# Optimization experiments

Measured on AMD Instinct MI355X. Metric: run time of the kernel, lower is better.

## Reference

```python
import jax, jax.numpy as jnp
import numpy as np

D_MODEL = 320
N_HEADS = 8
D_HEADS = 40
D_COND = 768
D_ATTN = N_HEADS * D_HEADS  # 320


def setup_inputs() -> dict:
    key = jax.random.key(0)
    ks = jax.random.split(key, 7)
    B, S, SK = 2, 4096, 4096
    x = jax.random.normal(ks[0], (B, S, D_MODEL), dtype=jnp.float32)
    cond = jax.random.normal(ks[1], (B, SK, D_COND), dtype=jnp.float32)
    # Linear weights stored as [in, out]; torch nn.Linear(in, out) has W [out, in],
    # applied as x @ W.T, equivalent to x @ W_here.
    sq = 1.0 / np.sqrt(D_MODEL)
    sc = 1.0 / np.sqrt(D_COND)
    sa = 1.0 / np.sqrt(D_ATTN)
    Wq = jax.random.uniform(ks[2], (D_MODEL, D_ATTN), jnp.float32, -sq, sq)
    Wk = jax.random.uniform(ks[3], (D_COND, D_ATTN), jnp.float32, -sc, sc)
    Wv = jax.random.uniform(ks[4], (D_COND, D_ATTN), jnp.float32, -sc, sc)
    Wo = jax.random.uniform(ks[5], (D_ATTN, D_MODEL), jnp.float32, -sa, sa)
    bo = jax.random.uniform(ks[6], (D_MODEL,), jnp.float32, -sa, sa)
    return {"x": x, "cond": cond, "Wq": Wq, "Wk": Wk, "Wv": Wv, "Wo": Wo, "bo": bo}


def reference(x, cond, Wq, Wk, Wv, Wo, bo):
    B, S, _ = x.shape
    SK = cond.shape[1]
    scale = D_HEADS ** -0.5
    q = (x @ Wq).reshape(B, S, N_HEADS, D_HEADS)      # [B,S,H,Dh]
    k = (cond @ Wk).reshape(B, SK, N_HEADS, D_HEADS)  # [B,SK,H,Dh]
    v = (cond @ Wv).reshape(B, SK, N_HEADS, D_HEADS)
    # materialized O(N^2) scores, as in the source (einsum -> softmax -> einsum)
    attn = jnp.einsum('bihd,bjhd->bhij', q, k) * scale  # [B,H,S,SK]
    attn = jax.nn.softmax(attn, axis=-1)
    out = jnp.einsum('bhij,bjhd->bihd', attn, v)        # [B,S,H,Dh]
    out = out.reshape(B, S, D_ATTN)
    return out @ Wo + bo
```

## Files before the change

### kernel.cpp

```cpp
#include <hip/hip_runtime.h>

typedef __attribute__((ext_vector_type(8))) short s16x8;
typedef __attribute__((ext_vector_type(4))) short s16x4;
typedef __attribute__((ext_vector_type(8))) __bf16 bf16x8;
typedef __attribute__((ext_vector_type(4))) float f32x4;
typedef __attribute__((ext_vector_type(4))) unsigned short u16x4;
typedef __attribute__((ext_vector_type(4))) unsigned int u32x4;

__device__ __forceinline__ f32x4 mfma_bf16(s16x8 a, s16x8 b, f32x4 c) {
  return __builtin_amdgcn_mfma_f32_16x16x32_bf16(
      __builtin_bit_cast(bf16x8, a), __builtin_bit_cast(bf16x8, b), c, 0, 0, 0);
}

__device__ __forceinline__ unsigned short f2bf(float f) {
  unsigned int u = __builtin_bit_cast(unsigned int, f);
  unsigned int r = u + 0x7FFFu + ((u >> 16) & 1u);
  return (unsigned short)(r >> 16);
}

__device__ __forceinline__ unsigned int cvt_pk_bf16(float lo, float hi) {
  unsigned int d;
  asm volatile("v_cvt_pk_bf16_f32 %0, %1, %2" : "=v"(d) : "v"(lo), "v"(hi));
  return d;
}

__global__ __launch_bounds__(256) void f32_to_bf16(const float* __restrict__ in,
                                                   unsigned short* __restrict__ out,
                                                   int n4) {
  int i = blockIdx.x * 256 + threadIdx.x;
  if (i < n4) {
    f32x4 v = ((const f32x4*)in)[i];
    u16x4 o;
    o[0] = f2bf(v[0]); o[1] = f2bf(v[1]); o[2] = f2bf(v[2]); o[3] = f2bf(v[3]);
    ((u16x4*)out)[i] = o;
  }
}

__global__ void transpose_f32_bf16(const float* __restrict__ in,
                                   unsigned short* __restrict__ out, int K, int N) {
  int id = blockIdx.x * 256 + threadIdx.x;
  if (id < K * N) {
    int k = id / N, n = id - k * N;
    out[(size_t)n * K + k] = f2bf(in[id]);
  }
}

template <int MODE, int K>
__global__ __launch_bounds__(256) void gemm_direct(
    const unsigned short* __restrict__ A, const unsigned short* __restrict__ Wt,
    void* __restrict__ dstv, const float* __restrict__ bias, float scale) {
  const int tid = threadIdx.x;
  const int l = tid & 63, w = tid >> 6;
  const int wm = w >> 1, wn = w & 1;
  const int lr = l & 15, lg = l >> 4;
  const int row0 = blockIdx.x * 64 + wm * 32;
  const int col0 = blockIdx.y * 64 + wn * 32;

  const unsigned short* Ap = A + (size_t)(row0 + lr) * K + lg * 8;
  const unsigned short* Bp = Wt + (size_t)(col0 + lr) * K + lg * 8;

  f32x4 acc[2][2];
#pragma unroll
  for (int i = 0; i < 2; i++)
#pragma unroll
    for (int j = 0; j < 2; j++) acc[i][j] = f32x4{0.f, 0.f, 0.f, 0.f};

  constexpr int NB = K / 32;
  s16x8 a0[2], a1[2], b0[2], b1[2];
  a0[0] = *(const s16x8*)(Ap);
  a1[0] = *(const s16x8*)(Ap + (size_t)16 * K);
  b0[0] = *(const s16x8*)(Bp);
  b1[0] = *(const s16x8*)(Bp + (size_t)16 * K);

#pragma unroll
  for (int i = 0; i < NB; i++) {
    const int cur = i & 1, nxt = cur ^ 1;
    if (i + 1 < NB) {
      const int k = (i + 1) * 32;
      a0[nxt] = *(const s16x8*)(Ap + k);
      a1[nxt] = *(const s16x8*)(Ap + (size_t)16 * K + k);
      b0[nxt] = *(const s16x8*)(Bp + k);
      b1[nxt] = *(const s16x8*)(Bp + (size_t)16 * K + k);
    }
    acc[0][0] = mfma_bf16(a0[cur], b0[cur], acc[0][0]);
    acc[0][1] = mfma_bf16(a0[cur], b1[cur], acc[0][1]);
    acc[1][0] = mfma_bf16(a1[cur], b0[cur], acc[1][0]);
    acc[1][1] = mfma_bf16(a1[cur], b1[cur], acc[1][1]);
  }

#pragma unroll
  for (int mf = 0; mf < 2; mf++)
#pragma unroll
    for (int nf = 0; nf < 2; nf++)
#pragma unroll
      for (int r = 0; r < 4; r++) {
        int m = row0 + mf * 16 + lg * 4 + r;
        int n = col0 + nf * 16 + lr;
        float v = acc[mf][nf][r];
        if (MODE == 0 || MODE == 1) {
          int b = m >> 12, s = m & 4095;
          int h = n / 40, d = n - h * 40;
          ((unsigned short*)dstv)[((size_t)(b * 8 + h) * 4096 + s) * 64 + d] =
              f2bf(v * scale);
        } else if (MODE == 2) {
          int b = m >> 12, s = m & 4095;
          int h = n / 40, d = n - h * 40;
          ((unsigned short*)dstv)[((size_t)(b * 8 + h) * 48 + d) * 4096 + s] = f2bf(v);
        } else {
          ((float*)dstv)[(size_t)m * 320 + n] = v + bias[n];
        }
      }
}

__global__ __launch_bounds__(512) void attn_kernel(
    const unsigned short* __restrict__ Qh, const unsigned short* __restrict__ Kh,
    const unsigned short* __restrict__ Vt, unsigned short* __restrict__ AO) {
  __shared__ __align__(16) char kt[8192];
  __shared__ __align__(16) char vts[6144];

  const int tid = threadIdx.x;
  const int l = tid & 63, w = tid >> 6;
  const int lr = l & 15, lg = l >> 4;
  const int bh = blockIdx.y;
  const int b = bh >> 3, h = bh & 7;
  const int qbase = blockIdx.x * 128;
  const int qrow = qbase + w * 16 + lr;

  const unsigned short* Qp = Qh + ((size_t)bh * 4096 + qbase + w * 16) * 64;
  const unsigned short* Kp = Kh + (size_t)bh * 4096 * 64;
  const unsigned short* Vp = Vt + (size_t)bh * 48 * 4096;

  const int srow = tid >> 3, sch = tid & 7;
  const bool hasv = (tid < 384);
  const int kofs = ((srow * 128 + sch * 16) ^ ((srow & 7) << 4));

  s16x8 q0 = *(const s16x8*)(Qp + lr * 64 + lg * 8);
  s16x8 q1 = *(const s16x8*)(Qp + lr * 64 + 32 + lg * 8);

  f32x4 O[3];
#pragma unroll
  for (int nf = 0; nf < 3; nf++) O[nf] = f32x4{0.f, 0.f, 0.f, 0.f};
  float rm = -1e30f, rl = 0.f;

  s16x8 kreg = *(const s16x8*)(Kp + (size_t)srow * 64 + sch * 8);
  s16x8 vreg;
  if (hasv) vreg = *(const s16x8*)(Vp + (size_t)srow * 4096 + sch * 8);
  *(s16x8*)(kt + kofs) = kreg;
  if (hasv) *(s16x8*)(vts + kofs) = vreg;
  __syncthreads();

  for (int kb = 0; kb < 4096; kb += 64) {
    if (kb + 64 < 4096) {
      kreg = *(const s16x8*)(Kp + (size_t)(kb + 64 + srow) * 64 + sch * 8);
      if (hasv) vreg = *(const s16x8*)(Vp + (size_t)srow * 4096 + kb + 64 + sch * 8);
    }

    f32x4 sf[4];
#pragma unroll
    for (int nf = 0; nf < 4; nf++) sf[nf] = f32x4{0.f, 0.f, 0.f, 0.f};
    __builtin_amdgcn_s_setprio(1);
#pragma unroll
    for (int nf = 0; nf < 4; nf++) {
      int krow = nf * 16 + lr;
      s16x8 kf0 = *(const s16x8*)(kt + ((krow * 128 + lg * 16) ^ ((krow & 7) << 4)));
      s16x8 kf1 = *(const s16x8*)(kt + ((krow * 128 + 64 + lg * 16) ^ ((krow & 7) << 4)));
      sf[nf] = mfma_bf16(kf0, q0, sf[nf]);
      sf[nf] = mfma_bf16(kf1, q1, sf[nf]);
    }
    __builtin_amdgcn_s_setprio(0);

    float tm = fmaxf(fmaxf(fmaxf(sf[0][0], sf[0][1]), fmaxf(sf[0][2], sf[0][3])),
                     fmaxf(fmaxf(sf[1][0], sf[1][1]), fmaxf(sf[1][2], sf[1][3])));
    tm = fmaxf(tm, fmaxf(fmaxf(fmaxf(sf[2][0], sf[2][1]), fmaxf(sf[2][2], sf[2][3])),
                         fmaxf(fmaxf(sf[3][0], sf[3][1]), fmaxf(sf[3][2], sf[3][3]))));
    tm = fmaxf(tm, __shfl_xor(tm, 16, 64));
    tm = fmaxf(tm, __shfl_xor(tm, 32, 64));
    if (!__all(tm <= rm)) {
      float mn = fmaxf(rm, tm);
      float al = __builtin_amdgcn_exp2f(rm - mn);
      rm = mn;
      rl *= al;
#pragma unroll
      for (int nf = 0; nf < 3; nf++) {
#pragma unroll
        for (int r = 0; r < 4; r++) O[nf][r] *= al;
      }
    }
    float ts = 0.f;
    unsigned int pk[4][2];
#pragma unroll
    for (int nf = 0; nf < 4; nf++) {
      float p0 = __builtin_amdgcn_exp2f(sf[nf][0] - rm);
      float p1 = __builtin_amdgcn_exp2f(sf[nf][1] - rm);
      float p2 = __builtin_amdgcn_exp2f(sf[nf][2] - rm);
      float p3 = __builtin_amdgcn_exp2f(sf[nf][3] - rm);
      ts += (p0 + p1) + (p2 + p3);
      pk[nf][0] = cvt_pk_bf16(p0, p1);
      pk[nf][1] = cvt_pk_bf16(p2, p3);
    }
    ts += __shfl_xor(ts, 16, 64);
    ts += __shfl_xor(ts, 32, 64);
    rl += ts;

    __builtin_amdgcn_s_setprio(1);
#pragma unroll
    for (int c = 0; c < 2; c++) {
      u32x4 bu = {pk[2 * c][0], pk[2 * c][1], pk[2 * c + 1][0], pk[2 * c + 1][1]};
      s16x8 bfrag = __builtin_bit_cast(s16x8, bu);
#pragma unroll
      for (int nf = 0; nf < 3; nf++) {
        int row = nf * 16 + lr;
        int base = row * 128 + c * 64 + lg * 8;
        int swz = (row & 7) << 4;
        s16x4 a0 = *(const s16x4*)(vts + ((base) ^ swz));
        s16x4 a1 = *(const s16x4*)(vts + ((base + 32) ^ swz));
        s16x8 afrag = {a0[0], a0[1], a0[2], a0[3], a1[0], a1[1], a1[2], a1[3]};
        O[nf] = mfma_bf16(afrag, bfrag, O[nf]);
      }
    }
    __builtin_amdgcn_s_setprio(0);

    __syncthreads();
    if (kb + 64 < 4096) {
      *(s16x8*)(kt + kofs) = kreg;
      if (hasv) *(s16x8*)(vts + kofs) = vreg;
    }
    __syncthreads();
  }

  float inv = 1.f / rl;
#pragma unroll
  for (int nf = 0; nf < 3; nf++) {
#pragma unroll
    for (int r = 0; r < 4; r++) {
      int d = nf * 16 + lg * 4 + r;
      if (d < 40) {
        AO[((size_t)(b * 4096 + qrow)) * 320 + h * 40 + d] = f2bf(O[nf][r] * inv);
      }
    }
  }
}

extern "C" void kernel_launch(void* const* d_in, const int* in_sizes, int n_in,
                              void* d_out, int out_size, void* d_ws,
                              size_t ws_size, hipStream_t stream) {
  const float* x    = (const float*)d_in[0];
  const float* cond = (const float*)d_in[1];
  const float* Wq   = (const float*)d_in[2];
  const float* Wk   = (const float*)d_in[3];
  const float* Wv   = (const float*)d_in[4];
  const float* Wo   = (const float*)d_in[5];
  const float* bo   = (const float*)d_in[6];

  char* ws = (char*)d_ws;
  unsigned short* xb    = (unsigned short*)(ws + 0);
  unsigned short* condb = (unsigned short*)(ws + 5242880);
  unsigned short* WtQ   = (unsigned short*)(ws + 17825792);
  unsigned short* WtK   = (unsigned short*)(ws + 18030592);
  unsigned short* WtV   = (unsigned short*)(ws + 18522112);
  unsigned short* WtO   = (unsigned short*)(ws + 19013632);
  unsigned short* AO    = (unsigned short*)(ws + 19218432);
  unsigned short* Qh    = (unsigned short*)(ws + 24461312);
  unsigned short* Kh    = (unsigned short*)(ws + 32849920);
  unsigned short* Vt    = (unsigned short*)(ws + 41238528);

  hipMemsetAsync(Qh, 0, 23068672, stream);

  f32_to_bf16<<<dim3(2560), 256, 0, stream>>>(x, xb, 655360);
  f32_to_bf16<<<dim3(6144), 256, 0, stream>>>(cond, condb, 1572864);

  transpose_f32_bf16<<<dim3(400), 256, 0, stream>>>(Wq, WtQ, 320, 320);
  transpose_f32_bf16<<<dim3(960), 256, 0, stream>>>(Wk, WtK, 768, 320);
  transpose_f32_bf16<<<dim3(960), 256, 0, stream>>>(Wv, WtV, 768, 320);
  transpose_f32_bf16<<<dim3(400), 256, 0, stream>>>(Wo, WtO, 320, 320);

  const float qscale = 1.44269504088896f / sqrtf(40.0f);

  gemm_direct<0, 320><<<dim3(128, 5), 256, 0, stream>>>(xb, WtQ, Qh, nullptr, qscale);
  gemm_direct<1, 768><<<dim3(128, 5), 256, 0, stream>>>(condb, WtK, Kh, nullptr, 1.0f);
  gemm_direct<2, 768><<<dim3(128, 5), 256, 0, stream>>>(condb, WtV, Vt, nullptr, 1.0f);

  attn_kernel<<<dim3(32, 16), 512, 0, stream>>>(Qh, Kh, Vt, AO);

  gemm_direct<3, 320><<<dim3(128, 5), 256, 0, stream>>>(AO, WtO, d_out, bo, 1.0f);
}
```

Measured before the change: 294.9 us.

## Double-buffer attention K/V tiles, permute V layout, and merge small launches

The attention loop now ping-pongs between two LDS buffers for K and V, so the next tile is written while the current one is read, and each iteration needs one barrier instead of two. V columns are stored in a permuted sequence order so the PV operand loads as a single 16-byte LDS read rather than two 8-byte reads plus a shuffle. The conversion, transpose and Q/K/V projection kernels are each merged into single launches to cut launch overhead. LDS use doubles per block, and the sequence permutation must match the P fragment order exactly.

```diff
diff --git a/kernel.cpp b/kernel.cpp
--- a/kernel.cpp
+++ b/kernel.cpp
@@ -1,7 +1,6 @@
 #include <hip/hip_runtime.h>
 
 typedef __attribute__((ext_vector_type(8))) short s16x8;
-typedef __attribute__((ext_vector_type(4))) short s16x4;
 typedef __attribute__((ext_vector_type(8))) __bf16 bf16x8;
 typedef __attribute__((ext_vector_type(4))) float f32x4;
 typedef __attribute__((ext_vector_type(4))) unsigned short u16x4;
@@ -24,29 +23,45 @@
   return d;
 }
 
-__global__ __launch_bounds__(256) void f32_to_bf16(const float* __restrict__ in,
-                                                   unsigned short* __restrict__ out,
-                                                   int n4) {
+__global__ __launch_bounds__(256) void convert_all(const float* __restrict__ x,
+                                                   const float* __restrict__ cond,
+                                                   unsigned short* __restrict__ xb,
+                                                   unsigned short* __restrict__ condb) {
   int i = blockIdx.x * 256 + threadIdx.x;
-  if (i < n4) {
-    f32x4 v = ((const f32x4*)in)[i];
-    u16x4 o;
-    o[0] = f2bf(v[0]); o[1] = f2bf(v[1]); o[2] = f2bf(v[2]); o[3] = f2bf(v[3]);
-    ((u16x4*)out)[i] = o;
+  const float* in;
+  unsigned short* out;
+  if (i < 655360) {
+    in = x; out = xb;
+  } else {
+    i -= 655360;
+    if (i >= 1572864) return;
+    in = cond; out = condb;
   }
-}
-
-__global__ void transpose_f32_bf16(const float* __restrict__ in,
-                                   unsigned short* __restrict__ out, int K, int N) {
+  f32x4 v = ((const f32x4*)in)[i];
+  u16x4 o;
+  o[0] = f2bf(v[0]); o[1] = f2bf(v[1]); o[2] = f2bf(v[2]); o[3] = f2bf(v[3]);
+  ((u16x4*)out)[i] = o;
+}
+
+__global__ void transpose_all(const float* __restrict__ Wq, const float* __restrict__ Wk,
+                              const float* __restrict__ Wv, const float* __restrict__ Wo,
+                              unsigned short* __restrict__ WtQ, unsigned short* __restrict__ WtK,
+                              unsigned short* __restrict__ WtV, unsigned short* __restrict__ WtO) {
   int id = blockIdx.x * 256 + threadIdx.x;
-  if (id < K * N) {
-    int k = id / N, n = id - k * N;
-    out[(size_t)n * K + k] = f2bf(in[id]);
-  }
+  const float* in;
+  unsigned short* out;
+  int K;
+  if (id < 102400)      { in = Wq; out = WtQ; K = 320; }
+  else if (id < 348160) { in = Wk; out = WtK; K = 768; id -= 102400; }
+  else if (id < 593920) { in = Wv; out = WtV; K = 768; id -= 348160; }
+  else if (id < 696320) { in = Wo; out = WtO; K = 320; id -= 593920; }
+  else return;
+  int k = id / 320, n = id - k * 320;
+  out[(size_t)n * K + k] = f2bf(in[id]);
 }
 
 template <int MODE, int K>
-__global__ __launch_bounds__(256) void gemm_direct(
+__device__ __forceinline__ void gemm_body(
     const unsigned short* __restrict__ A, const unsigned short* __restrict__ Wt,
     void* __restrict__ dstv, const float* __restrict__ bias, float scale) {
   const int tid = threadIdx.x;
@@ -105,18 +120,35 @@
         } else if (MODE == 2) {
           int b = m >> 12, s = m & 4095;
           int h = n / 40, d = n - h * 40;
-          ((unsigned short*)dstv)[((size_t)(b * 8 + h) * 48 + d) * 4096 + s] = f2bf(v);
+          int sp = (s & ~63) | (s & 35) | ((s & 12) << 1) | ((s & 16) >> 2);
+          ((unsigned short*)dstv)[((size_t)(b * 8 + h) * 48 + d) * 4096 + sp] = f2bf(v);
         } else {
           ((float*)dstv)[(size_t)m * 320 + n] = v + bias[n];
         }
       }
 }
 
+__global__ __launch_bounds__(256) void qkv_proj(
+    const unsigned short* __restrict__ xb, const unsigned short* __restrict__ condb,
+    const unsigned short* __restrict__ WtQ, const unsigned short* __restrict__ WtK,
+    const unsigned short* __restrict__ WtV, unsigned short* __restrict__ Qh,
+    unsigned short* __restrict__ Kh, unsigned short* __restrict__ Vt, float qscale) {
+  if (blockIdx.z == 0)      gemm_body<0, 320>(xb, WtQ, Qh, nullptr, qscale);
+  else if (blockIdx.z == 1) gemm_body<1, 768>(condb, WtK, Kh, nullptr, 1.0f);
+  else                      gemm_body<2, 768>(condb, WtV, Vt, nullptr, 1.0f);
+}
+
+__global__ __launch_bounds__(256) void o_proj(
+    const unsigned short* __restrict__ AO, const unsigned short* __restrict__ WtO,
+    float* __restrict__ out, const float* __restrict__ bias) {
+  gemm_body<3, 320>(AO, WtO, out, bias, 1.0f);
+}
+
 __global__ __launch_bounds__(512) void attn_kernel(
     const unsigned short* __restrict__ Qh, const unsigned short* __restrict__ Kh,
     const unsigned short* __restrict__ Vt, unsigned short* __restrict__ AO) {
-  __shared__ __align__(16) char kt[8192];
-  __shared__ __align__(16) char vts[6144];
+  __shared__ __align__(16) char kt[2][8192];
+  __shared__ __align__(16) char vts[2][6144];
 
   const int tid = threadIdx.x;
   const int l = tid & 63, w = tid >> 6;
@@ -145,12 +177,17 @@
   s16x8 kreg = *(const s16x8*)(Kp + (size_t)srow * 64 + sch * 8);
   s16x8 vreg;
   if (hasv) vreg = *(const s16x8*)(Vp + (size_t)srow * 4096 + sch * 8);
-  *(s16x8*)(kt + kofs) = kreg;
-  if (hasv) *(s16x8*)(vts + kofs) = vreg;
+  *(s16x8*)(kt[0] + kofs) = kreg;
+  if (hasv) *(s16x8*)(vts[0] + kofs) = vreg;
   __syncthreads();
 
-  for (int kb = 0; kb < 4096; kb += 64) {
-    if (kb + 64 < 4096) {
+  for (int t = 0; t < 64; ++t) {
+    const int kb = t * 64;
+    const int p = t & 1;
+    const char* ktp = kt[p];
+    const char* vtp = vts[p];
+
+    if (t + 1 < 64) {
       kreg = *(const s16x8*)(Kp + (size_t)(kb + 64 + srow) * 64 + sch * 8);
       if (hasv) vreg = *(const s16x8*)(Vp + (size_t)srow * 4096 + kb + 64 + sch * 8);
     }
@@ -162,8 +199,8 @@
 #pragma unroll
     for (int nf = 0; nf < 4; nf++) {
       int krow = nf * 16 + lr;
-      s16x8 kf0 = *(const s16x8*)(kt + ((krow * 128 + lg * 16) ^ ((krow & 7) << 4)));
-      s16x8 kf1 = *(const s16x8*)(kt + ((krow * 128 + 64 + lg * 16) ^ ((krow & 7) << 4)));
+      s16x8 kf0 = *(const s16x8*)(ktp + ((krow * 128 + lg * 16) ^ ((krow & 7) << 4)));
+      s16x8 kf1 = *(const s16x8*)(ktp + ((krow * 128 + 64 + lg * 16) ^ ((krow & 7) << 4)));
       sf[nf] = mfma_bf16(kf0, q0, sf[nf]);
       sf[nf] = mfma_bf16(kf1, q1, sf[nf]);
     }
@@ -210,22 +247,18 @@
 #pragma unroll
       for (int nf = 0; nf < 3; nf++) {
         int row = nf * 16 + lr;
-        int base = row * 128 + c * 64 + lg * 8;
-        int swz = (row & 7) << 4;
-        s16x4 a0 = *(const s16x4*)(vts + ((base) ^ swz));
-        s16x4 a1 = *(const s16x4*)(vts + ((base + 32) ^ swz));
-        s16x8 afrag = {a0[0], a0[1], a0[2], a0[3], a1[0], a1[1], a1[2], a1[3]};
+        s16x8 afrag = *(const s16x8*)(
+            vtp + ((row * 128 + c * 64 + lg * 16) ^ ((row & 7) << 4)));
         O[nf] = mfma_bf16(afrag, bfrag, O[nf]);
       }
     }
     __builtin_amdgcn_s_setprio(0);
 
-    __syncthreads();
-    if (kb + 64 < 4096) {
-      *(s16x8*)(kt + kofs) = kreg;
-      if (hasv) *(s16x8*)(vts + kofs) = vreg;
-    }
-    __syncthreads();
+    if (t + 1 < 64) {
+      *(s16x8*)(kt[p ^ 1] + kofs) = kreg;
+      if (hasv) *(s16x8*)(vts[p ^ 1] + kofs) = vreg;
+      __syncthreads();
+    }
   }
 
   float inv = 1.f / rl;
@@ -266,21 +299,13 @@
 
   hipMemsetAsync(Qh, 0, 23068672, stream);
 
-  f32_to_bf16<<<dim3(2560), 256, 0, stream>>>(x, xb, 655360);
-  f32_to_bf16<<<dim3(6144), 256, 0, stream>>>(cond, condb, 1572864);
-
-  transpose_f32_bf16<<<dim3(400), 256, 0, stream>>>(Wq, WtQ, 320, 320);
-  transpose_f32_bf16<<<dim3(960), 256, 0, stream>>>(Wk, WtK, 768, 320);
-  transpose_f32_bf16<<<dim3(960), 256, 0, stream>>>(Wv, WtV, 768, 320);
-  transpose_f32_bf16<<<dim3(400), 256, 0, stream>>>(Wo, WtO, 320, 320);
+  convert_all<<<dim3(8704), 256, 0, stream>>>(x, cond, xb, condb);
+  transpose_all<<<dim3(2720), 256, 0, stream>>>(Wq, Wk, Wv, Wo, WtQ, WtK, WtV, WtO);
 
   const float qscale = 1.44269504088896f / sqrtf(40.0f);
 
-  gemm_direct<0, 320><<<dim3(128, 5), 256, 0, stream>>>(xb, WtQ, Qh, nullptr, qscale);
-  gemm_direct<1, 768><<<dim3(128, 5), 256, 0, stream>>>(condb, WtK, Kh, nullptr, 1.0f);
-  gemm_direct<2, 768><<<dim3(128, 5), 256, 0, stream>>>(condb, WtV, Vt, nullptr, 1.0f);
-
+  qkv_proj<<<dim3(128, 5, 3), 256, 0, stream>>>(xb, condb, WtQ, WtK, WtV, Qh, Kh, Vt,
+                                                qscale);
   attn_kernel<<<dim3(32, 16), 512, 0, stream>>>(Qh, Kh, Vt, AO);
-
-  gemm_direct<3, 320><<<dim3(128, 5), 256, 0, stream>>>(AO, WtO, d_out, bo, 1.0f);
-}
+  o_proj<<<dim3(128, 5), 256, 0, stream>>>(AO, WtO, (float*)d_out, bo);
+}
```

New measurement: 274.5 us. 6.9% less time.
